# Performance work log

Measured on AMD Instinct MI355X. Metric: run time of the kernel, lower is better.

Reference implementation:

```python
import jax, jax.numpy as jnp
import numpy as np

N = 40000        # total nodes (2000 graphs x 20 nodes)
E = 60000        # edges per relation (before self-loops)
R = 6            # number of relations
IN = 32
HID = 128
OUT = 128
H = 2            # heads
C = 128          # per-head out channels (concat=False)
B = 2000         # number of graphs
NEG_SLOPE = 0.2


def setup_inputs() -> dict:
    key = jax.random.key(0)
    ks = jax.random.split(key, 16)
    rn = lambda k, s, sc=0.05: (jax.random.normal(k, s, jnp.float32) * sc)
    x = jax.random.normal(ks[0], (N, IN), jnp.float32)
    edge_index = jax.random.randint(ks[1], (R, 2, E), 0, N, dtype=jnp.int32)
    batch = (jnp.arange(N, dtype=jnp.int32) // (N // B)).astype(jnp.int32)
    return {
        "x": x, "edge_index": edge_index, "batch": batch,
        "Wl1": rn(ks[2], (R, IN, H * C)), "bl1": jnp.zeros((R, H * C), jnp.float32),
        "Wr1": rn(ks[3], (R, IN, H * C)), "br1": jnp.zeros((R, H * C), jnp.float32),
        "att1": rn(ks[4], (R, H, C)), "bias1": jnp.zeros((R, C), jnp.float32),
        "Wl2": rn(ks[5], (R, HID, H * C)), "bl2": jnp.zeros((R, H * C), jnp.float32),
        "Wr2": rn(ks[6], (R, HID, H * C)), "br2": jnp.zeros((R, H * C), jnp.float32),
        "att2": rn(ks[7], (R, H, C)), "bias2": jnp.zeros((R, C), jnp.float32),
        "ln1_g": jnp.ones((HID,), jnp.float32), "ln1_b": jnp.zeros((HID,), jnp.float32),
        "ln2_g": jnp.ones((HID,), jnp.float32), "ln2_b": jnp.zeros((HID,), jnp.float32),
        "query": rn(ks[8], (HID,), 0.02),
        "projW": rn(ks[9], (HID, OUT)), "projb": jnp.zeros((OUT,), jnp.float32),
    }


def _gatv2(x, src, dst, Wl, bl, Wr, br, att, bias):
    # x: [N, F]; src/dst: [Etot] (self-loops already appended)
    n = x.shape[0]
    xl = (x @ Wl + bl).reshape(n, H, C)   # source transform
    xr = (x @ Wr + br).reshape(n, H, C)   # target transform
    e = jax.nn.leaky_relu(xl[src] + xr[dst], NEG_SLOPE)   # [Etot, H, C]
    logits = jnp.einsum('ehc,hc->eh', e, att)             # [Etot, H]
    m = jax.ops.segment_max(logits, dst, num_segments=n)
    a = jnp.exp(logits - m[dst])
    s = jax.ops.segment_sum(a, dst, num_segments=n)
    w = a / s[dst]                                        # segment softmax
    out = jax.ops.segment_sum(w[:, :, None] * xl[src], dst, num_segments=n)
    return out.mean(axis=1) + bias                        # head-average (concat=False)


def _hetero_layer(x, edge_index, Wl, bl, Wr, br, att, bias):
    loops = jnp.broadcast_to(jnp.arange(N, dtype=edge_index.dtype), (R, N))
    src = jnp.concatenate([edge_index[:, 0, :], loops], axis=1)  # [R, E+N]
    dst = jnp.concatenate([edge_index[:, 1, :], loops], axis=1)
    outs = jax.vmap(_gatv2, in_axes=(None, 0, 0, 0, 0, 0, 0, 0, 0))(
        x, src, dst, Wl, bl, Wr, br, att, bias)
    return outs.sum(axis=0)  # HeteroConv aggr='sum'


def _layernorm(x, g, b, eps=1e-5):
    mu = x.mean(-1, keepdims=True)
    var = ((x - mu) ** 2).mean(-1, keepdims=True)
    return (x - mu) * jax.lax.rsqrt(var + eps) * g + b


def reference(x, edge_index, batch, Wl1, bl1, Wr1, br1, att1, bias1,
              Wl2, bl2, Wr2, br2, att2, bias2,
              ln1_g, ln1_b, ln2_g, ln2_b, query, projW, projb):
    h = _hetero_layer(x, edge_index, Wl1, bl1, Wr1, br1, att1, bias1)
    h = _layernorm(jnp.tanh(h), ln1_g, ln1_b)
    h = _hetero_layer(h, edge_index, Wl2, bl2, Wr2, br2, att2, bias2)
    h = _layernorm(jnp.tanh(h), ln2_g, ln2_b)
    # attention pooling over graphs (segment softmax on batch ids)
    scores = h @ query                              # [N]
    m = jax.ops.segment_max(scores, batch, num_segments=B)
    a = jnp.exp(scores - m[batch])
    s = jax.ops.segment_sum(a, batch, num_segments=B)
    w = a / s[batch]
    g = jax.ops.segment_sum(w[:, None] * h, batch, num_segments=B)  # [B, HID]
    return g @ projW + projb
```

## Files before the change

kernel.cpp:

```cpp
#include <hip/hip_runtime.h>
#include <hip/hip_bf16.h>
#include <math.h>

#define N_NODES 40000
#define E_EDGES 60000
#define R_REL 6
#define IN_F 32
#define HID_F 128
#define B_GRAPHS 2000
#define NODES_PER_G 20
#define NEG_SLOPE 0.2f
#define NB (R_REL * N_NODES)
#define NTOT (R_REL * (E_EDGES + N_NODES))
#define NBLK ((NB + 255) / 256)

typedef __bf16 bf16x8 __attribute__((ext_vector_type(8)));
typedef float f32x4 __attribute__((ext_vector_type(4)));

__device__ __forceinline__ unsigned f2bfbits(float f) {
    unsigned u = __builtin_bit_cast(unsigned, f);
    return (u + 0x7FFFu + ((u >> 16) & 1u)) >> 16;
}
__device__ __forceinline__ float bflo(unsigned u) { return __builtin_bit_cast(float, u << 16); }
__device__ __forceinline__ float bfhi(unsigned u) { return __builtin_bit_cast(float, u & 0xFFFF0000u); }

__global__ __launch_bounds__(256) void count_kernel(
    const int* __restrict__ ei, int* __restrict__ cnt)
{
    int idx = blockIdx.x * 256 + threadIdx.x;
    if (idx >= NTOT) return;
    int bin;
    if (idx < R_REL * E_EDGES) {
        int r = idx / E_EDGES, e = idx - r * E_EDGES;
        bin = r * N_NODES + ei[(size_t)r * 2 * E_EDGES + E_EDGES + e];
    } else {
        bin = idx - R_REL * E_EDGES;
    }
    atomicAdd(&cnt[bin], 1);
}

__global__ __launch_bounds__(256) void scan1_kernel(
    const int* __restrict__ cnt, int* __restrict__ part, int* __restrict__ bsum)
{
    int i = blockIdx.x * 256 + threadIdx.x;
    int v = (i < NB) ? cnt[i] : 0;
    int lane = threadIdx.x & 63, w = threadIdx.x >> 6;
    int x = v;
#pragma unroll
    for (int off = 1; off < 64; off <<= 1) {
        int y = __shfl_up(x, off, 64);
        if (lane >= off) x += y;
    }
    __shared__ int ws[4];
    if (lane == 63) ws[w] = x;
    __syncthreads();
    int add = 0;
    for (int j = 0; j < w; j++) add += ws[j];
    int incl = x + add;
    if (i < NB) part[i] = incl - v;
    if (threadIdx.x == 255) bsum[blockIdx.x] = incl;
}

__global__ __launch_bounds__(1024) void scan2_kernel(
    const int* __restrict__ bsum, int* __restrict__ boff)
{
    __shared__ int buf[1024];
    int t = threadIdx.x;
    int v0 = (t < NBLK) ? bsum[t] : 0;
    buf[t] = v0;
    __syncthreads();
    for (int off = 1; off < 1024; off <<= 1) {
        int v = (t >= off) ? buf[t - off] : 0;
        __syncthreads();
        buf[t] += v;
        __syncthreads();
    }
    if (t < NBLK) boff[t] = buf[t] - v0;
}

__global__ __launch_bounds__(256) void scan3_kernel(
    const int* __restrict__ part, const int* __restrict__ boff,
    int* __restrict__ rowptr, int* __restrict__ cursor)
{
    int i = blockIdx.x * 256 + threadIdx.x;
    if (i < NB) {
        int v = part[i] + boff[i >> 8];
        rowptr[i] = v;
        cursor[i] = v;
    }
    if (i == 0) rowptr[NB] = NTOT;
}

__global__ __launch_bounds__(256) void scatter_kernel(
    const int* __restrict__ ei, int* __restrict__ cursor, int* __restrict__ csr)
{
    int idx = blockIdx.x * 256 + threadIdx.x;
    if (idx >= NTOT) return;
    int bin, src;
    if (idx < R_REL * E_EDGES) {
        int r = idx / E_EDGES, e = idx - r * E_EDGES;
        src = ei[(size_t)r * 2 * E_EDGES + e];
        bin = r * N_NODES + ei[(size_t)r * 2 * E_EDGES + E_EDGES + e];
    } else {
        bin = idx - R_REL * E_EDGES;
        src = bin % N_NODES;
    }
    int pos = atomicAdd(&cursor[bin], 1);
    csr[pos] = src;
}

__global__ __launch_bounds__(256) void cvt_bf16_kernel(
    const float* __restrict__ src, unsigned* __restrict__ dst, int npairs)
{
    int i = blockIdx.x * 256 + threadIdx.x;
    if (i >= npairs) return;
    float2 v = *(const float2*)(src + 2 * i);
    dst[i] = f2bfbits(v.x) | (f2bfbits(v.y) << 16);
}

__global__ __launch_bounds__(256) void prep_w_kernel(
    const float* __restrict__ Wl, const float* __restrict__ Wr,
    const float* __restrict__ bl, const float* __restrict__ br,
    unsigned short* __restrict__ Bt, float* __restrict__ bcat, int K)
{
    int idx = blockIdx.x * 256 + threadIdx.x;
    if (idx >= R_REL * 512 * K) return;
    int k = idx % K;
    int rn = idx / K;
    int n = rn % 512;
    int r = rn / 512;
    int nn = n & 255;
    const float* W = (n < 256) ? Wl : Wr;
    float w = W[((size_t)r * K + k) * 256 + nn];
    Bt[idx] = (unsigned short)f2bfbits(w);
    if (k == 0)
        bcat[rn] = (n < 256) ? bl[r * 256 + nn] : br[r * 256 + nn];
}

template <int K, int ZPB>
__global__ __launch_bounds__(256) void gemm_mfma_kernel(
    const unsigned short* __restrict__ A,
    const unsigned short* __restrict__ BtAll,
    const float* __restrict__ biasAll,
    unsigned short* __restrict__ CAll)
{
    constexpr int CHUNKS = K / 8;
    constexpr int ABYTES = 128 * K * 2;
    __shared__ char lds[ABYTES + 16384];
    char* ldsA = lds;
    char* ldsB = lds + ABYTES;

    int tid = threadIdx.x;
    int lane = tid & 63, wave = tid >> 6;
    int l16 = lane & 15, quad = lane >> 4;
    int wm = (wave >> 1) * 64, wn = (wave & 1) * 64;
    int m0 = blockIdx.x * 128, n0 = blockIdx.y * 128;
    int zbase = blockIdx.z * ZPB;

#pragma unroll
    for (int it = 0; it < (128 * CHUNKS) / 256; ++it) {
        int s = it * 256 + tid;
        int row = s / CHUNKS, sc = s % CHUNKS;
        int sw = (K == 128) ? (row & 7) : ((row >> 1) & 3);
        int c = sc ^ sw;
        int gr = m0 + row; gr = gr < N_NODES ? gr : N_NODES - 1;
        const char* gp = (const char*)A + (size_t)gr * (K * 2) + c * 16;
        __builtin_amdgcn_global_load_lds(
            (const __attribute__((address_space(1))) void*)gp,
            (__attribute__((address_space(3))) void*)(ldsA + it * 4096 + wave * 1024), 16, 0, 0);
    }

    auto stageB = [&](int z, int k0, int pb) {
        const char* Bt = (const char*)(BtAll + (size_t)(zbase + z) * 512 * K);
#pragma unroll
        for (int it = 0; it < 2; ++it) {
            int s = it * 256 + tid;
            int row = s >> 2, sc = s & 3;
            int c = sc ^ ((row >> 1) & 3);
            const char* gp = Bt + (size_t)(n0 + row) * (K * 2) + k0 * 2 + c * 16;
            __builtin_amdgcn_global_load_lds(
                (const __attribute__((address_space(1))) void*)gp,
                (__attribute__((address_space(3))) void*)(ldsB + pb * 8192 + it * 4096 + wave * 1024), 16, 0, 0);
        }
    };

    stageB(0, 0, 0);
    __syncthreads();

    int p = 0;
    for (int z = 0; z < ZPB; ++z) {
        f32x4 acc[4][4];
#pragma unroll
        for (int i = 0; i < 4; i++)
#pragma unroll
            for (int j = 0; j < 4; j++) {
                acc[i][j][0] = 0.f; acc[i][j][1] = 0.f;
                acc[i][j][2] = 0.f; acc[i][j][3] = 0.f;
            }

        for (int k0 = 0; k0 < K; k0 += 32) {
            int nz = (k0 + 32 < K) ? z : z + 1;
            int nk = (k0 + 32 < K) ? k0 + 32 : 0;
            if (nz < ZPB) stageB(nz, nk, p ^ 1);

            bf16x8 af[4], bfr[4];
#pragma unroll
            for (int i = 0; i < 4; i++) {
                int row = wm + i * 16 + l16;
                int sw = (K == 128) ? (row & 7) : ((row >> 1) & 3);
                int c = (k0 / 8 + quad) ^ sw;
                af[i] = *(const bf16x8*)(ldsA + row * (K * 2) + c * 16);
            }
#pragma unroll
            for (int j = 0; j < 4; j++) {
                int row = wn + j * 16 + l16;
                int c = quad ^ ((row >> 1) & 3);
                bfr[j] = *(const bf16x8*)(ldsB + p * 8192 + row * 64 + c * 16);
            }
#pragma unroll
            for (int i = 0; i < 4; i++)
#pragma unroll
                for (int j = 0; j < 4; j++)
                    acc[i][j] = __builtin_amdgcn_mfma_f32_16x16x32_bf16(af[i], bfr[j], acc[i][j], 0, 0, 0);
            __syncthreads();
            p ^= 1;
        }

        const float* bias = biasAll + (zbase + z) * 512;
        unsigned short* C = CAll + (size_t)(zbase + z) * N_NODES * 512;
        float biasj[4];
#pragma unroll
        for (int j = 0; j < 4; j++) biasj[j] = bias[n0 + wn + j * 16 + l16];
#pragma unroll
        for (int i = 0; i < 4; i++) {
            int gr0 = m0 + wm + i * 16 + quad * 4;
#pragma unroll
            for (int j = 0; j < 4; j++) {
                int col = n0 + wn + j * 16 + l16;
#pragma unroll
                for (int rg = 0; rg < 4; rg++) {
                    float a = acc[i][j][rg] + biasj[j];
                    float b = __shfl_xor(a, 1);
                    int grow = gr0 + rg;
                    if (!(lane & 1) && grow < N_NODES) {
                        __hip_bfloat162 h2 = __float22bfloat162_rn(make_float2(a, b));
                        unsigned u;
                        __builtin_memcpy(&u, &h2, 4);
                        *(unsigned*)((char*)C + ((size_t)grow * 512 + col) * 2) = u;
                    }
                }
            }
        }
    }
}

__global__ __launch_bounds__(256) void gat6_ln_kernel(
    const unsigned short* __restrict__ XLR,
    const int* __restrict__ rowptr,
    const int* __restrict__ csr,
    const float* __restrict__ att,
    const float* __restrict__ bias,
    const float* __restrict__ lng, const float* __restrict__ lnb,
    unsigned* __restrict__ hout)
{
    int gtid = blockIdx.x * 256 + threadIdx.x;
    int d = gtid >> 6;
    int lane = threadIdx.x & 63;
    if (d >= N_NODES) return;
    int hl = lane & 31;

    float tot0 = 0.f, tot1 = 0.f, tot2 = 0.f, tot3 = 0.f;
#pragma unroll 1
    for (int r = 0; r < R_REL; r++) {
        const char* base = (const char*)XLR + (size_t)r * N_NODES * 1024;
        const unsigned* xrp = (const unsigned*)(base + (size_t)d * 1024 + 512 + lane * 8);
        unsigned xu0 = xrp[0], xu1 = xrp[1];
        float xr0 = bflo(xu0), xr1 = bfhi(xu0), xr2 = bflo(xu1), xr3 = bfhi(xu1);
        float4 av = *(const float4*)(att + r * 256 + lane * 4);

        int bin = r * N_NODES + d;
        int beg = __builtin_amdgcn_readfirstlane(rowptr[bin]);
        int end = __builtin_amdgcn_readfirstlane(rowptr[bin + 1]);

        float sA = 0.f, a0 = 0.f, a1 = 0.f, a2 = 0.f, a3 = 0.f;
        float sB = 0.f, b0 = 0.f, b1 = 0.f, b2 = 0.f, b3 = 0.f;
        int i = beg;
        for (; i + 2 <= end; i += 2) {
            int s0 = csr[i], s1 = csr[i + 1];
            const unsigned* pA = (const unsigned*)(base + (size_t)s0 * 1024 + lane * 8);
            const unsigned* pB = (const unsigned*)(base + (size_t)s1 * 1024 + lane * 8);
            unsigned uA0 = pA[0], uA1 = pA[1];
            unsigned uB0 = pB[0], uB1 = pB[1];
            float xA0 = bflo(uA0), xA1 = bfhi(uA0), xA2 = bflo(uA1), xA3 = bfhi(uA1);
            float xB0 = bflo(uB0), xB1 = bfhi(uB0), xB2 = bflo(uB1), xB3 = bfhi(uB1);
            float tA0 = xA0 + xr0, tA1 = xA1 + xr1, tA2 = xA2 + xr2, tA3 = xA3 + xr3;
            float tB0 = xB0 + xr0, tB1 = xB1 + xr1, tB2 = xB2 + xr2, tB3 = xB3 + xr3;
            tA0 = fmaxf(tA0, NEG_SLOPE * tA0); tB0 = fmaxf(tB0, NEG_SLOPE * tB0);
            tA1 = fmaxf(tA1, NEG_SLOPE * tA1); tB1 = fmaxf(tB1, NEG_SLOPE * tB1);
            tA2 = fmaxf(tA2, NEG_SLOPE * tA2); tB2 = fmaxf(tB2, NEG_SLOPE * tB2);
            tA3 = fmaxf(tA3, NEG_SLOPE * tA3); tB3 = fmaxf(tB3, NEG_SLOPE * tB3);
            float pa = tA0 * av.x + tA1 * av.y + tA2 * av.z + tA3 * av.w;
            float pb = tB0 * av.x + tB1 * av.y + tB2 * av.z + tB3 * av.w;
            pa += __shfl_xor(pa, 16); pb += __shfl_xor(pb, 16);
            pa += __shfl_xor(pa, 8);  pb += __shfl_xor(pb, 8);
            pa += __shfl_xor(pa, 4);  pb += __shfl_xor(pb, 4);
            pa += __shfl_xor(pa, 2);  pb += __shfl_xor(pb, 2);
            pa += __shfl_xor(pa, 1);  pb += __shfl_xor(pb, 1);
            float wa = __expf(fminf(pa, 60.f));
            float wb = __expf(fminf(pb, 60.f));
            sA += wa; sB += wb;
            a0 = fmaf(wa, xA0, a0); b0 = fmaf(wb, xB0, b0);
            a1 = fmaf(wa, xA1, a1); b1 = fmaf(wb, xB1, b1);
            a2 = fmaf(wa, xA2, a2); b2 = fmaf(wb, xB2, b2);
            a3 = fmaf(wa, xA3, a3); b3 = fmaf(wb, xB3, b3);
        }
        if (i < end) {
            int s0 = csr[i];
            const unsigned* pA = (const unsigned*)(base + (size_t)s0 * 1024 + lane * 8);
            unsigned uA0 = pA[0], uA1 = pA[1];
            float xA0 = bflo(uA0), xA1 = bfhi(uA0), xA2 = bflo(uA1), xA3 = bfhi(uA1);
            float tA0 = xA0 + xr0, tA1 = xA1 + xr1, tA2 = xA2 + xr2, tA3 = xA3 + xr3;
            tA0 = fmaxf(tA0, NEG_SLOPE * tA0);
            tA1 = fmaxf(tA1, NEG_SLOPE * tA1);
            tA2 = fmaxf(tA2, NEG_SLOPE * tA2);
            tA3 = fmaxf(tA3, NEG_SLOPE * tA3);
            float pa = tA0 * av.x + tA1 * av.y + tA2 * av.z + tA3 * av.w;
            pa += __shfl_xor(pa, 16);
            pa += __shfl_xor(pa, 8);
            pa += __shfl_xor(pa, 4);
            pa += __shfl_xor(pa, 2);
            pa += __shfl_xor(pa, 1);
            float wa = __expf(fminf(pa, 60.f));
            sA += wa;
            a0 = fmaf(wa, xA0, a0);
            a1 = fmaf(wa, xA1, a1);
            a2 = fmaf(wa, xA2, a2);
            a3 = fmaf(wa, xA3, a3);
        }
        sA += sB; a0 += b0; a1 += b1; a2 += b2; a3 += b3;
        float rs = 0.5f * __builtin_amdgcn_rcpf(sA);
        float o0 = a0 * rs, o1 = a1 * rs, o2 = a2 * rs, o3 = a3 * rs;
        o0 += __shfl_xor(o0, 32);
        o1 += __shfl_xor(o1, 32);
        o2 += __shfl_xor(o2, 32);
        o3 += __shfl_xor(o3, 32);
        float4 bv = *(const float4*)(bias + r * 128 + hl * 4);
        tot0 += o0 + bv.x;
        tot1 += o1 + bv.y;
        tot2 += o2 + bv.z;
        tot3 += o3 + bv.w;
    }
    float v0 = tanhf(tot0), v1 = tanhf(tot1), v2 = tanhf(tot2), v3 = tanhf(tot3);
    float sum = v0 + v1 + v2 + v3;
    float sq = v0 * v0 + v1 * v1 + v2 * v2 + v3 * v3;
#pragma unroll
    for (int off = 16; off >= 1; off >>= 1) {
        sum += __shfl_xor(sum, off);
        sq  += __shfl_xor(sq, off);
    }
    float mean = sum * (1.f / 128.f);
    float var = sq * (1.f / 128.f) - mean * mean;
    float rstd = rsqrtf(var + 1e-5f);
    float4 gg = *(const float4*)(lng + hl * 4);
    float4 bb = *(const float4*)(lnb + hl * 4);
    float o0 = (v0 - mean) * rstd * gg.x + bb.x;
    float o1 = (v1 - mean) * rstd * gg.y + bb.y;
    float o2 = (v2 - mean) * rstd * gg.z + bb.z;
    float o3 = (v3 - mean) * rstd * gg.w + bb.w;
    if (lane < 32) {
        uint2 q;
        q.x = f2bfbits(o0) | (f2bfbits(o1) << 16);
        q.y = f2bfbits(o2) | (f2bfbits(o3) << 16);
        *((uint2*)(hout + (size_t)d * 64) + hl) = q;
    }
}

__global__ __launch_bounds__(256) void pool_kernel(
    const unsigned* __restrict__ hb, const float* __restrict__ query,
    float* __restrict__ gout)
{
    int gtid = blockIdx.x * 256 + threadIdx.x;
    int bg = gtid >> 6;
    int lane = threadIdx.x & 63;
    if (bg >= B_GRAPHS) return;
    float2 q = *(const float2*)(query + 2 * lane);
    float mx = -1e30f, ssum = 0.f, g0 = 0.f, g1 = 0.f;
    for (int i = 0; i < NODES_PER_G; i++) {
        unsigned u = hb[(size_t)(bg * NODES_PER_G + i) * 64 + lane];
        float h0 = bflo(u), h1 = bfhi(u);
        float p = h0 * q.x + h1 * q.y;
#pragma unroll
        for (int off = 32; off >= 1; off >>= 1) p += __shfl_xor(p, off, 64);
        float mn = fmaxf(mx, p);
        float sc = __expf(mx - mn), w = __expf(p - mn);
        ssum = ssum * sc + w;
        g0 = g0 * sc + w * h0;
        g1 = g1 * sc + w * h1;
        mx = mn;
    }
    float2 o; o.x = g0 / ssum; o.y = g1 / ssum;
    *(float2*)(gout + (size_t)bg * 128 + 2 * lane) = o;
}

__global__ __launch_bounds__(128) void proj_kernel(
    const float* __restrict__ g, const float* __restrict__ W,
    const float* __restrict__ bias, float* __restrict__ out)
{
    int bg = blockIdx.x;
    int o = threadIdx.x;
    const float* gp = g + (size_t)bg * 128;
    float acc = bias[o];
    for (int k = 0; k < 128; k++) acc = fmaf(gp[k], W[k * 128 + o], acc);
    out[(size_t)bg * 128 + o] = acc;
}

extern "C" void kernel_launch(void* const* d_in, const int* in_sizes, int n_in,
                              void* d_out, int out_size, void* d_ws, size_t ws_size,
                              hipStream_t stream)
{
    const float* x     = (const float*)d_in[0];
    const int*   ei    = (const int*)d_in[1];
    const float* Wl1   = (const float*)d_in[3];
    const float* bl1   = (const float*)d_in[4];
    const float* Wr1   = (const float*)d_in[5];
    const float* br1   = (const float*)d_in[6];
    const float* att1  = (const float*)d_in[7];
    const float* bias1 = (const float*)d_in[8];
    const float* Wl2   = (const float*)d_in[9];
    const float* bl2   = (const float*)d_in[10];
    const float* Wr2   = (const float*)d_in[11];
    const float* br2   = (const float*)d_in[12];
    const float* att2  = (const float*)d_in[13];
    const float* bias2 = (const float*)d_in[14];
    const float* ln1g  = (const float*)d_in[15];
    const float* ln1b  = (const float*)d_in[16];
    const float* ln2g  = (const float*)d_in[17];
    const float* ln2b  = (const float*)d_in[18];
    const float* query = (const float*)d_in[19];
    const float* projW = (const float*)d_in[20];
    const float* projb = (const float*)d_in[21];
    float* out = (float*)d_out;

    unsigned short* xlr6 = (unsigned short*)d_ws;
    unsigned short* h1bf = xlr6 + (size_t)R_REL * N_NODES * 512;
    unsigned short* xbf  = h1bf + (size_t)N_NODES * 128;
    unsigned short* Bt1  = xbf + (size_t)N_NODES * 32;
    unsigned short* Bt2  = Bt1 + R_REL * 512 * 32;
    float* bc1  = (float*)(Bt2 + R_REL * 512 * 128);
    float* bc2  = bc1 + R_REL * 512;
    float* gb   = bc2 + R_REL * 512;
    int* cnt    = (int*)(gb + (size_t)B_GRAPHS * 128);
    int* part   = cnt + NB;
    int* rowptr = part + NB;
    int* cursor = rowptr + NB + 1;
    int* bsum   = cursor + NB;
    int* boff   = bsum + NBLK;
    int* csr    = boff + NBLK;

    hipMemsetAsync(cnt, 0, sizeof(int) * NB, stream);
    count_kernel<<<(NTOT + 255) / 256, 256, 0, stream>>>(ei, cnt);
    scan1_kernel<<<NBLK, 256, 0, stream>>>(cnt, part, bsum);
    scan2_kernel<<<1, 1024, 0, stream>>>(bsum, boff);
    scan3_kernel<<<NBLK, 256, 0, stream>>>(part, boff, rowptr, cursor);
    scatter_kernel<<<(NTOT + 255) / 256, 256, 0, stream>>>(ei, cursor, csr);

    cvt_bf16_kernel<<<(N_NODES * 16 + 255) / 256, 256, 0, stream>>>(x, (unsigned*)xbf, N_NODES * 16);
    prep_w_kernel<<<(R_REL * 512 * 32 + 255) / 256, 256, 0, stream>>>(Wl1, Wr1, bl1, br1, Bt1, bc1, 32);
    prep_w_kernel<<<(R_REL * 512 * 128 + 255) / 256, 256, 0, stream>>>(Wl2, Wr2, bl2, br2, Bt2, bc2, 128);

    dim3 g1((N_NODES + 127) / 128, 4, 1);
    gemm_mfma_kernel<32, 6><<<g1, 256, 0, stream>>>(xbf, Bt1, bc1, xlr6);
    gat6_ln_kernel<<<N_NODES / 4, 256, 0, stream>>>(
        xlr6, rowptr, csr, att1, bias1, ln1g, ln1b, (unsigned*)h1bf);
    dim3 g2((N_NODES + 127) / 128, 4, 2);
    gemm_mfma_kernel<128, 3><<<g2, 256, 0, stream>>>(h1bf, Bt2, bc2, xlr6);
    gat6_ln_kernel<<<N_NODES / 4, 256, 0, stream>>>(
        xlr6, rowptr, csr, att2, bias2, ln2g, ln2b, (unsigned*)h1bf);
    pool_kernel<<<B_GRAPHS / 4, 256, 0, stream>>>((unsigned*)h1bf, query, gb);
    proj_kernel<<<B_GRAPHS, 128, 0, stream>>>(gb, projW, projb, out);
}
```

Before: 479.9 us.

## Keep A fragments in registers, stage full B tile, and coalesce epilogue stores via LDS

The GEMM now loads the full-K B tile for each relation in one stage instead of double-buffering 32-wide K slices. A fragments are held in registers across all relations, so they are read from LDS once. Per-k-step barriers are removed, leaving one sync per relation. The epilogue stages the bf16 outputs through a per-wave swizzled LDS scratch and writes 16-byte coalesced rows instead of scattered 4-byte stores. The cost is more LDS per block and extra registers for the held fragments, which may lower occupancy, and the next B load is no longer overlapped with the MFMAs.

```diff
diff --git a/kernel.cpp b/kernel.cpp
--- a/kernel.cpp
+++ b/kernel.cpp
@@ -144,11 +144,12 @@
     const float* __restrict__ biasAll,
     unsigned short* __restrict__ CAll)
 {
-    constexpr int CHUNKS = K / 8;
-    constexpr int ABYTES = 128 * K * 2;
-    __shared__ char lds[ABYTES + 16384];
+    constexpr int CH = K / 8;
+    constexpr int TBYTES = 128 * K * 2;
+    __shared__ char lds[2 * TBYTES + 16384];
     char* ldsA = lds;
-    char* ldsB = lds + ABYTES;
+    char* ldsB = lds + TBYTES;
+    char* ldsS = lds + 2 * TBYTES;
 
     int tid = threadIdx.x;
     int lane = tid & 63, wave = tid >> 6;
@@ -157,12 +158,13 @@
     int m0 = blockIdx.x * 128, n0 = blockIdx.y * 128;
     int zbase = blockIdx.z * ZPB;
 
-#pragma unroll
-    for (int it = 0; it < (128 * CHUNKS) / 256; ++it) {
+    auto SW = [](int row) { return (K == 128) ? (row & 7) : ((row >> 1) & 3); };
+
+#pragma unroll
+    for (int it = 0; it < K / 16; ++it) {
         int s = it * 256 + tid;
-        int row = s / CHUNKS, sc = s % CHUNKS;
-        int sw = (K == 128) ? (row & 7) : ((row >> 1) & 3);
-        int c = sc ^ sw;
+        int row = s / CH, sc = s % CH;
+        int c = sc ^ SW(row);
         int gr = m0 + row; gr = gr < N_NODES ? gr : N_NODES - 1;
         const char* gp = (const char*)A + (size_t)gr * (K * 2) + c * 16;
         __builtin_amdgcn_global_load_lds(
@@ -170,25 +172,38 @@
             (__attribute__((address_space(3))) void*)(ldsA + it * 4096 + wave * 1024), 16, 0, 0);
     }
 
-    auto stageB = [&](int z, int k0, int pb) {
+    auto stageB = [&](int z) {
         const char* Bt = (const char*)(BtAll + (size_t)(zbase + z) * 512 * K);
 #pragma unroll
-        for (int it = 0; it < 2; ++it) {
+        for (int it = 0; it < K / 16; ++it) {
             int s = it * 256 + tid;
-            int row = s >> 2, sc = s & 3;
-            int c = sc ^ ((row >> 1) & 3);
-            const char* gp = Bt + (size_t)(n0 + row) * (K * 2) + k0 * 2 + c * 16;
+            int row = s / CH, sc = s % CH;
+            int c = sc ^ SW(row);
+            const char* gp = Bt + (size_t)(n0 + row) * (K * 2) + c * 16;
             __builtin_amdgcn_global_load_lds(
                 (const __attribute__((address_space(1))) void*)gp,
-                (__attribute__((address_space(3))) void*)(ldsB + pb * 8192 + it * 4096 + wave * 1024), 16, 0, 0);
+                (__attribute__((address_space(3))) void*)(ldsB + it * 4096 + wave * 1024), 16, 0, 0);
         }
     };
 
-    stageB(0, 0, 0);
+    stageB(0);
     __syncthreads();
 
-    int p = 0;
+    bf16x8 afr[K / 32][4];
+#pragma unroll
+    for (int kk = 0; kk < K / 32; ++kk)
+#pragma unroll
+        for (int i = 0; i < 4; ++i) {
+            int row = wm + i * 16 + l16;
+            int slot = (kk * 4 + quad) ^ SW(row);
+            afr[kk][i] = *(const bf16x8*)(ldsA + row * (K * 2) + slot * 16);
+        }
+
+    char* myS = ldsS + wave * 4096;
+
     for (int z = 0; z < ZPB; ++z) {
+        if (z) __syncthreads();
+
         f32x4 acc[4][4];
 #pragma unroll
         for (int i = 0; i < 4; i++)
@@ -198,57 +213,67 @@
                 acc[i][j][2] = 0.f; acc[i][j][3] = 0.f;
             }
 
-        for (int k0 = 0; k0 < K; k0 += 32) {
-            int nz = (k0 + 32 < K) ? z : z + 1;
-            int nk = (k0 + 32 < K) ? k0 + 32 : 0;
-            if (nz < ZPB) stageB(nz, nk, p ^ 1);
-
-            bf16x8 af[4], bfr[4];
-#pragma unroll
-            for (int i = 0; i < 4; i++) {
-                int row = wm + i * 16 + l16;
-                int sw = (K == 128) ? (row & 7) : ((row >> 1) & 3);
-                int c = (k0 / 8 + quad) ^ sw;
-                af[i] = *(const bf16x8*)(ldsA + row * (K * 2) + c * 16);
+#pragma unroll
+        for (int kk = 0; kk < K / 32; ++kk) {
+            bf16x8 bfr[4];
+#pragma unroll
+            for (int j = 0; j < 4; ++j) {
+                int row = wn + j * 16 + l16;
+                int slot = (kk * 4 + quad) ^ SW(row);
+                bfr[j] = *(const bf16x8*)(ldsB + row * (K * 2) + slot * 16);
             }
 #pragma unroll
-            for (int j = 0; j < 4; j++) {
-                int row = wn + j * 16 + l16;
-                int c = quad ^ ((row >> 1) & 3);
-                bfr[j] = *(const bf16x8*)(ldsB + p * 8192 + row * 64 + c * 16);
-            }
-#pragma unroll
             for (int i = 0; i < 4; i++)
 #pragma unroll
                 for (int j = 0; j < 4; j++)
-                    acc[i][j] = __builtin_amdgcn_mfma_f32_16x16x32_bf16(af[i], bfr[j], acc[i][j], 0, 0, 0);
-            __syncthreads();
-            p ^= 1;
+                    acc[i][j] = __builtin_amdgcn_mfma_f32_16x16x32_bf16(afr[kk][i], bfr[j], acc[i][j], 0, 0, 0);
         }
+        __syncthreads();
+        if (z + 1 < ZPB) stageB(z + 1);
 
         const float* bias = biasAll + (zbase + z) * 512;
         unsigned short* C = CAll + (size_t)(zbase + z) * N_NODES * 512;
         float biasj[4];
 #pragma unroll
-        for (int j = 0; j < 4; j++) biasj[j] = bias[n0 + wn + j * 16 + l16];
-#pragma unroll
-        for (int i = 0; i < 4; i++) {
-            int gr0 = m0 + wm + i * 16 + quad * 4;
-#pragma unroll
-            for (int j = 0; j < 4; j++) {
-                int col = n0 + wn + j * 16 + l16;
-#pragma unroll
-                for (int rg = 0; rg < 4; rg++) {
-                    float a = acc[i][j][rg] + biasj[j];
-                    float b = __shfl_xor(a, 1);
-                    int grow = gr0 + rg;
-                    if (!(lane & 1) && grow < N_NODES) {
-                        __hip_bfloat162 h2 = __float22bfloat162_rn(make_float2(a, b));
-                        unsigned u;
-                        __builtin_memcpy(&u, &h2, 4);
-                        *(unsigned*)((char*)C + ((size_t)grow * 512 + col) * 2) = u;
-                    }
+        for (int j = 0; j < 4; ++j) biasj[j] = bias[n0 + wn + j * 16 + l16];
+
+        int par = lane & 1;
+#pragma unroll
+        for (int half = 0; half < 2; ++half) {
+#pragma unroll
+            for (int i2 = 0; i2 < 2; ++i2) {
+                int i = half * 2 + i2;
+#pragma unroll
+                for (int j = 0; j < 4; ++j) {
+                    float a0 = acc[i][j][0] + biasj[j];
+                    float a1 = acc[i][j][1] + biasj[j];
+                    float a2 = acc[i][j][2] + biasj[j];
+                    float a3 = acc[i][j][3] + biasj[j];
+                    float b0 = __shfl_xor(a0, 1);
+                    float b1 = __shfl_xor(a1, 1);
+                    float b2 = __shfl_xor(a2, 1);
+                    float b3 = __shfl_xor(a3, 1);
+                    float lo0 = par ? b2 : a0, hi0 = par ? a2 : b0;
+                    float lo1 = par ? b3 : a1, hi1 = par ? a3 : b1;
+                    __hip_bfloat162 h0 = __float22bfloat162_rn(make_float2(lo0, hi0));
+                    __hip_bfloat162 h1 = __float22bfloat162_rn(make_float2(lo1, hi1));
+                    unsigned u0, u1;
+                    __builtin_memcpy(&u0, &h0, 4);
+                    __builtin_memcpy(&u1, &h1, 4);
+                    int r0 = i2 * 16 + quad * 4 + par * 2;
+                    int dcol = (j * 8 + (l16 >> 1)) ^ (quad * 8);
+                    *(unsigned*)(myS + r0 * 128 + dcol * 4) = u0;
+                    *(unsigned*)(myS + (r0 + 1) * 128 + dcol * 4) = u1;
                 }
+            }
+#pragma unroll
+            for (int t = 0; t < 4; ++t) {
+                int rr = t * 8 + (lane >> 3);
+                int db = ((lane & 7) * 4) ^ (((rr >> 2) & 3) * 8);
+                uint4 v = *(const uint4*)(myS + rr * 128 + db * 4);
+                int grow = m0 + wm + half * 32 + rr;
+                if (grow < N_NODES)
+                    *(uint4*)((char*)C + ((size_t)grow * 512 + n0 + wn) * 2 + (lane & 7) * 16) = v;
             }
         }
     }
```

Measured after the change: 484.0 us. Within noise of the previous version (+0.9%).
